# Kernel tuning notes

Hardware: AMD Instinct MI355X
Metric: run time of the kernel (lower is better)

The kernel has to match this reference:

```python
import jax, jax.numpy as jnp
import numpy as np


def setup_inputs() -> dict:
    key = jax.random.key(0)
    kq, kk, kv, km = jax.random.split(key, 4)
    B, H, S, D = 2, 16, 2048, 64
    q = jax.random.normal(kq, (B, H, S, D), dtype=jnp.float32)
    k = jax.random.normal(kk, (B, H, S, D), dtype=jnp.float32)
    v = jax.random.normal(kv, (B, H, S, D), dtype=jnp.float32)
    mask = jax.random.randint(km, (B, 1, S, D * S // D), 0, 2).astype(bool)
    return {"q": q, "k": k, "v": v, "mask": mask, "d_k": 64}


def reference(q, k, v, mask, d_k):
    # score = q @ k^T / sqrt(d_k), masked_fill(mask, -1e9)
    scale = jnp.float32(1.0 / np.sqrt(d_k))
    score = jnp.einsum("bhsd,bhtd->bhst", q, k) * scale  # [B,H,S,S]
    score = jnp.where(mask, jnp.float32(-1e9), score)
    attention = jax.nn.softmax(score, axis=-1)
    # NOTE: original module (faithfully) multiplies the RAW masked score by v,
    # not the softmaxed attention: results = score @ v
    results = jnp.einsum("bhst,bhtd->bhsd", score, v)
    return (results, attention)
```

## Files before the change

kernel.cpp:

```cpp
#include <hip/hip_runtime.h>

typedef __attribute__((ext_vector_type(8))) short short8;
typedef __attribute__((ext_vector_type(4))) float f32x4;

#define S_LEN 2048
#define DH 64

__device__ __forceinline__ unsigned short f2bf(float x) {
  unsigned u = __builtin_bit_cast(unsigned, x);
  u += 0x7fffu + ((u >> 16) & 1u);
  return (unsigned short)(u >> 16);
}

__global__ void detect_stride_k(const unsigned char* __restrict__ m, int* flag) {
  __shared__ int any;
  if (threadIdx.x == 0) any = 0;
  __syncthreads();
  int acc = 0;
  for (int i = threadIdx.x; i < 4096; i += 256)
    if (i & 3) acc |= m[i];
  if (acc) atomicOr(&any, 1);
  __syncthreads();
  if (threadIdx.x == 0) *flag = any ? 1 : 4;
}

__global__ void pack_mask_k(const unsigned char* __restrict__ m,
                            const int* __restrict__ flagp,
                            unsigned* __restrict__ bits) {
  int idx = blockIdx.x * 256 + threadIdx.x;
  unsigned w = 0;
  if (*flagp == 1) {
    const uint4* p = (const uint4*)(m + (size_t)idx * 32);
    uint4 a = p[0], bq = p[1];
    unsigned arr[8] = {a.x, a.y, a.z, a.w, bq.x, bq.y, bq.z, bq.w};
#pragma unroll
    for (int d = 0; d < 8; ++d)
#pragma unroll
      for (int j = 0; j < 4; ++j)
        w |= (((arr[d] >> (8 * j)) & 255u) != 0u ? 1u : 0u) << (d * 4 + j);
  } else {
    const uint4* p = (const uint4*)m + (size_t)idx * 8;
#pragma unroll
    for (int d = 0; d < 8; ++d) {
      uint4 v = p[d];
      w |= (v.x ? 1u : 0u) << (d * 4);
      w |= (v.y ? 1u : 0u) << (d * 4 + 1);
      w |= (v.z ? 1u : 0u) << (d * 4 + 2);
      w |= (v.w ? 1u : 0u) << (d * 4 + 3);
    }
  }
  bits[idx] = w;
}

__global__ void conv_k_kernel(const float* __restrict__ k, char* __restrict__ kbf) {
  int idx = blockIdx.x * 256 + threadIdx.x;
  const float4* s = (const float4*)k + (size_t)idx * 2;
  float4 a = s[0], b = s[1];
  int4 o;
  o.x = (int)f2bf(a.x) | ((int)f2bf(a.y) << 16);
  o.y = (int)f2bf(a.z) | ((int)f2bf(a.w) << 16);
  o.z = (int)f2bf(b.x) | ((int)f2bf(b.y) << 16);
  o.w = (int)f2bf(b.z) | ((int)f2bf(b.w) << 16);
  ((int4*)kbf)[idx] = o;
}

__global__ void trans_v_kernel(const float* __restrict__ v, char* __restrict__ vtbf) {
  int gt = blockIdx.x * 256 + threadIdx.x;
  int wid = gt >> 6;
  int lane = gt & 63;
  int bh = wid >> 9;
  int rem = wid & 511;
  int d0 = (rem >> 5) * 4;
  int t = (rem & 31) * 64 + lane;
  float4 val = *(const float4*)(v + ((size_t)bh * S_LEN + t) * DH + d0);
  unsigned short* o = (unsigned short*)vtbf;
  size_t base = ((size_t)bh * DH + d0) * S_LEN + t;
  o[base]             = f2bf(val.x);
  o[base + S_LEN]     = f2bf(val.y);
  o[base + 2 * S_LEN] = f2bf(val.z);
  o[base + 3 * S_LEN] = f2bf(val.w);
}

__global__ __launch_bounds__(512, 4)
void attn_fused(const float* __restrict__ qsrc,
                const unsigned* __restrict__ mbits,
                const char* __restrict__ kbf,
                const char* __restrict__ vtbf,
                float* __restrict__ out) {
  __shared__ __align__(16) char smem[81920];

  const int tid = threadIdx.x;
  const int lane = tid & 63;
  const int w = tid >> 6;
  const int l15 = lane & 15;
  const int g = lane >> 4;
  const int sw = (l15 & 7) << 4;

  int raw = blockIdx.x;
  int swz = (raw & 7) * 64 + (raw >> 3);
  const int bh = swz >> 4;
  const int qblk = swz & 15;
  const int b = bh >> 4;
  const int q0 = qblk * 128 + w * 16;

  const char* ksrc_bh = kbf + (size_t)bh * (S_LEN * DH * 2);
  const char* vsrc_bh = vtbf + (size_t)bh * (DH * S_LEN * 2);
  char* pb = smem + 65536 + w * 2048;

  const unsigned* mrow = mbits + (size_t)b * (S_LEN * (S_LEN / 32)) +
                         (size_t)(q0 + l15) * (S_LEN / 32);

  auto stageK = [&](int buf, int t0) {
    char* dst = smem + buf * 16384;
#pragma unroll
    for (int it = 0; it < 2; ++it) {
      int o = (w * 2 + it) * 1024 + lane * 16;
      int r = o >> 7;
      int inner = o & 127;
      const char* gp = ksrc_bh + (size_t)t0 * 128 + r * 128 + (inner ^ ((r & 7) << 4));
      __builtin_amdgcn_global_load_lds((const unsigned*)gp,
                                       (unsigned*)(dst + (w * 2 + it) * 1024), 16, 0, 0);
    }
  };
  auto stageV = [&](int buf, int t0) {
    char* dst = smem + 32768 + buf * 16384;
#pragma unroll
    for (int it = 0; it < 2; ++it) {
      int o = (w * 2 + it) * 1024 + lane * 16;
      int r = o >> 8;
      int inner = o & 255;
      const char* gp = vsrc_bh + (size_t)t0 * 2 + (size_t)r * (S_LEN * 2) +
                       (inner ^ ((r & 7) << 4));
      __builtin_amdgcn_global_load_lds((const unsigned*)gp,
                                       (unsigned*)(dst + (w * 2 + it) * 1024), 16, 0, 0);
    }
  };

  short8 qf[2];
#pragma unroll
  for (int kc = 0; kc < 2; ++kc) {
    const float* qp = qsrc + ((size_t)bh * S_LEN + q0 + l15) * DH + 32 * kc + 8 * g;
    float4 x = *(const float4*)qp;
    float4 y = *(const float4*)(qp + 4);
    short8 f;
    f[0] = (short)f2bf(x.x); f[1] = (short)f2bf(x.y);
    f[2] = (short)f2bf(x.z); f[3] = (short)f2bf(x.w);
    f[4] = (short)f2bf(y.x); f[5] = (short)f2bf(y.y);
    f[6] = (short)f2bf(y.z); f[7] = (short)f2bf(y.w);
    qf[kc] = f;
  }

  f32x4 acc[4];
#pragma unroll
  for (int i = 0; i < 4; ++i) acc[i] = (f32x4){0.f, 0.f, 0.f, 0.f};
  float lp = 0.f;

  stageK(0, 0);
  stageV(0, 0);
  uint4 mw = *(const uint4*)mrow;
  __syncthreads();
  int cur = 0;

  for (int t0 = 0; t0 < S_LEN; t0 += 128) {
    uint4 mw_n;
    if (t0 + 128 < S_LEN) {
      stageK(cur ^ 1, t0 + 128);
      stageV(cur ^ 1, t0 + 128);
      mw_n = *(const uint4*)(mrow + (t0 + 128) / 32);
    }
    const char* kbuf = smem + cur * 16384;
    const char* vbuf = smem + 32768 + cur * 16384;

    f32x4 sf[8];
#pragma unroll
    for (int tc = 0; tc < 8; ++tc) {
      const char* rowp = kbuf + (16 * tc + l15) * 128;
      short8 a0 = *(const short8*)(rowp + ((16 * g) ^ sw));
      short8 a1 = *(const short8*)(rowp + ((64 + 16 * g) ^ sw));
      f32x4 z = (f32x4){0.f, 0.f, 0.f, 0.f};
      f32x4 t00 = __builtin_amdgcn_mfma_f32_16x16x32_bf16(a0, qf[0], z, 0, 0, 0);
      sf[tc] = __builtin_amdgcn_mfma_f32_16x16x32_bf16(a1, qf[1], t00, 0, 0, 0);
    }

    const unsigned mwa[4] = {mw.x, mw.y, mw.z, mw.w};
#pragma unroll
    for (int h = 0; h < 2; ++h) {
      char* pbr = pb + l15 * 128;
#pragma unroll
      for (int tq = 0; tq < 4; ++tq) {
        const int tc = 4 * h + tq;
        unsigned nib = (mwa[tc >> 1] >> (16 * (tc & 1) + 4 * g)) & 15u;
        float s0 = (nib & 1u) ? -1e9f : sf[tc][0] * 0.125f;
        float s1 = (nib & 2u) ? -1e9f : sf[tc][1] * 0.125f;
        float s2 = (nib & 4u) ? -1e9f : sf[tc][2] * 0.125f;
        float s3 = (nib & 8u) ? -1e9f : sf[tc][3] * 0.125f;
        lp += __expf(s0) + __expf(s1) + __expf(s2) + __expf(s3);
        int2 pk;
        pk.x = (int)f2bf(s0) | ((int)f2bf(s1) << 16);
        pk.y = (int)f2bf(s2) | ((int)f2bf(s3) << 16);
        *(int2*)(pbr + ((32 * tq + 8 * g) ^ sw)) = pk;
      }
      short8 p0 = *(const short8*)(pb + l15 * 128 + ((16 * g) ^ sw));
      short8 p1 = *(const short8*)(pb + l15 * 128 + ((64 + 16 * g) ^ sw));
#pragma unroll
      for (int dr = 0; dr < 4; ++dr) {
        const char* vr = vbuf + (16 * dr + l15) * 256;
        short8 v0 = *(const short8*)(vr + ((h * 128 + 16 * g) ^ sw));
        short8 v1 = *(const short8*)(vr + ((h * 128 + 64 + 16 * g) ^ sw));
        acc[dr] = __builtin_amdgcn_mfma_f32_16x16x32_bf16(v0, p0, acc[dr], 0, 0, 0);
        acc[dr] = __builtin_amdgcn_mfma_f32_16x16x32_bf16(v1, p1, acc[dr], 0, 0, 0);
      }
    }

    mw = mw_n;
    __syncthreads();
    cur ^= 1;
  }

  float l = lp;
  l += __shfl_xor(l, 16);
  l += __shfl_xor(l, 32);
  const float inv = 1.0f / l;

#pragma unroll
  for (int dr = 0; dr < 4; ++dr) {
    float4 o;
    o.x = acc[dr][0]; o.y = acc[dr][1];
    o.z = acc[dr][2]; o.w = acc[dr][3];
    *(float4*)(out + ((size_t)bh * S_LEN + q0 + l15) * DH + 16 * dr + 4 * g) = o;
  }

  float* att = out + (size_t)4194304 + (size_t)bh * S_LEN * S_LEN;
  stageK(0, 0);
  mw = *(const uint4*)mrow;
  __syncthreads();
  cur = 0;

  for (int t0 = 0; t0 < S_LEN; t0 += 128) {
    uint4 mw_n;
    if (t0 + 128 < S_LEN) {
      stageK(cur ^ 1, t0 + 128);
      mw_n = *(const uint4*)(mrow + (t0 + 128) / 32);
    }
    const char* kbuf = smem + cur * 16384;

    const int q = q0 + l15;
    const unsigned mwa[4] = {mw.x, mw.y, mw.z, mw.w};
#pragma unroll
    for (int tc = 0; tc < 8; ++tc) {
      const char* rowp = kbuf + (16 * tc + l15) * 128;
      short8 a0 = *(const short8*)(rowp + ((16 * g) ^ sw));
      short8 a1 = *(const short8*)(rowp + ((64 + 16 * g) ^ sw));
      f32x4 z = (f32x4){0.f, 0.f, 0.f, 0.f};
      f32x4 t0f = __builtin_amdgcn_mfma_f32_16x16x32_bf16(a0, qf[0], z, 0, 0, 0);
      f32x4 sff = __builtin_amdgcn_mfma_f32_16x16x32_bf16(a1, qf[1], t0f, 0, 0, 0);
      const int t = t0 + 16 * tc + 4 * g;
      size_t eidx = (size_t)q * S_LEN + t;
      unsigned nib = (mwa[tc >> 1] >> (16 * (tc & 1) + 4 * g)) & 15u;
      float s0 = (nib & 1u) ? -1e9f : sff[0] * 0.125f;
      float s1 = (nib & 2u) ? -1e9f : sff[1] * 0.125f;
      float s2 = (nib & 4u) ? -1e9f : sff[2] * 0.125f;
      float s3 = (nib & 8u) ? -1e9f : sff[3] * 0.125f;
      float4 e;
      e.x = __expf(s0) * inv;
      e.y = __expf(s1) * inv;
      e.z = __expf(s2) * inv;
      e.w = __expf(s3) * inv;
      *(float4*)(att + eidx) = e;
    }

    mw = mw_n;
    __syncthreads();
    cur ^= 1;
  }
}

extern "C" void kernel_launch(void* const* d_in, const int* in_sizes, int n_in,
                              void* d_out, int out_size, void* d_ws, size_t ws_size,
                              hipStream_t stream) {
  (void)in_sizes; (void)n_in; (void)out_size; (void)ws_size;
  const float* q = (const float*)d_in[0];
  const float* k = (const float*)d_in[1];
  const float* v = (const float*)d_in[2];
  const unsigned char* mask = (const unsigned char*)d_in[3];
  float* out = (float*)d_out;

  char* ws = (char*)d_ws;
  int* flag = (int*)ws;
  char* kbf = ws + 256;
  char* vtbf = ws + 256 + 8 * 1024 * 1024;
  unsigned* bits = (unsigned*)(ws + 256 + 16 * 1024 * 1024);

  detect_stride_k<<<1, 256, 0, stream>>>(mask, flag);
  pack_mask_k<<<1024, 256, 0, stream>>>(mask, flag, bits);
  conv_k_kernel<<<2048, 256, 0, stream>>>(k, kbf);
  trans_v_kernel<<<4096, 256, 0, stream>>>(v, vtbf);
  attn_fused<<<512, 512, 0, stream>>>(q, bits, kbf, vtbf, out);
}
```

Before: 217.3 us.

## Merge prep kernels into one launch and read K directly in attention pass

Folds the K bf16 conversion, V transpose and mask bit-packing into one prep kernel, with the work split by block-index range, so two kernel launches go away. In the second (attention-writing) pass, K rows are now loaded straight from global/L2 instead of being double-buffered through shared memory, which removes the per-tile __syncthreads and LDS staging. The risk is that direct global loads of K, now without the swizzle, have higher latency and can stall the MFMA and store loop. The relies on `ksrc_bh` being defined in the hidden part of the kernel.

```diff
diff --git a/kernel.cpp b/kernel.cpp
--- a/kernel.cpp
+++ b/kernel.cpp
@@ -24,61 +24,64 @@
   if (threadIdx.x == 0) *flag = any ? 1 : 4;
 }
 
-__global__ void pack_mask_k(const unsigned char* __restrict__ m,
+__global__ void prep_kernel(const float* __restrict__ k,
+                            const float* __restrict__ v,
+                            const unsigned char* __restrict__ m,
                             const int* __restrict__ flagp,
+                            char* __restrict__ kbf,
+                            char* __restrict__ vtbf,
                             unsigned* __restrict__ bits) {
-  int idx = blockIdx.x * 256 + threadIdx.x;
-  unsigned w = 0;
-  if (*flagp == 1) {
-    const uint4* p = (const uint4*)(m + (size_t)idx * 32);
-    uint4 a = p[0], bq = p[1];
-    unsigned arr[8] = {a.x, a.y, a.z, a.w, bq.x, bq.y, bq.z, bq.w};
-#pragma unroll
-    for (int d = 0; d < 8; ++d)
-#pragma unroll
-      for (int j = 0; j < 4; ++j)
-        w |= (((arr[d] >> (8 * j)) & 255u) != 0u ? 1u : 0u) << (d * 4 + j);
+  int bid = blockIdx.x;
+  if (bid < 2048) {
+    int idx = bid * 256 + threadIdx.x;
+    const float4* s = (const float4*)k + (size_t)idx * 2;
+    float4 a = s[0], b = s[1];
+    int4 o;
+    o.x = (int)f2bf(a.x) | ((int)f2bf(a.y) << 16);
+    o.y = (int)f2bf(a.z) | ((int)f2bf(a.w) << 16);
+    o.z = (int)f2bf(b.x) | ((int)f2bf(b.y) << 16);
+    o.w = (int)f2bf(b.z) | ((int)f2bf(b.w) << 16);
+    ((int4*)kbf)[idx] = o;
+  } else if (bid < 6144) {
+    int gt = (bid - 2048) * 256 + threadIdx.x;
+    int wid = gt >> 6;
+    int lane = gt & 63;
+    int bh = wid >> 9;
+    int rem = wid & 511;
+    int d0 = (rem >> 5) * 4;
+    int t = (rem & 31) * 64 + lane;
+    float4 val = *(const float4*)(v + ((size_t)bh * S_LEN + t) * DH + d0);
+    unsigned short* o = (unsigned short*)vtbf;
+    size_t base = ((size_t)bh * DH + d0) * S_LEN + t;
+    o[base]             = f2bf(val.x);
+    o[base + S_LEN]     = f2bf(val.y);
+    o[base + 2 * S_LEN] = f2bf(val.z);
+    o[base + 3 * S_LEN] = f2bf(val.w);
   } else {
-    const uint4* p = (const uint4*)m + (size_t)idx * 8;
-#pragma unroll
-    for (int d = 0; d < 8; ++d) {
-      uint4 v = p[d];
-      w |= (v.x ? 1u : 0u) << (d * 4);
-      w |= (v.y ? 1u : 0u) << (d * 4 + 1);
-      w |= (v.z ? 1u : 0u) << (d * 4 + 2);
-      w |= (v.w ? 1u : 0u) << (d * 4 + 3);
-    }
-  }
-  bits[idx] = w;
-}
-
-__global__ void conv_k_kernel(const float* __restrict__ k, char* __restrict__ kbf) {
-  int idx = blockIdx.x * 256 + threadIdx.x;
-  const float4* s = (const float4*)k + (size_t)idx * 2;
-  float4 a = s[0], b = s[1];
-  int4 o;
-  o.x = (int)f2bf(a.x) | ((int)f2bf(a.y) << 16);
-  o.y = (int)f2bf(a.z) | ((int)f2bf(a.w) << 16);
-  o.z = (int)f2bf(b.x) | ((int)f2bf(b.y) << 16);
-  o.w = (int)f2bf(b.z) | ((int)f2bf(b.w) << 16);
-  ((int4*)kbf)[idx] = o;
-}
-
-__global__ void trans_v_kernel(const float* __restrict__ v, char* __restrict__ vtbf) {
-  int gt = blockIdx.x * 256 + threadIdx.x;
-  int wid = gt >> 6;
-  int lane = gt & 63;
-  int bh = wid >> 9;
-  int rem = wid & 511;
-  int d0 = (rem >> 5) * 4;
-  int t = (rem & 31) * 64 + lane;
-  float4 val = *(const float4*)(v + ((size_t)bh * S_LEN + t) * DH + d0);
-  unsigned short* o = (unsigned short*)vtbf;
-  size_t base = ((size_t)bh * DH + d0) * S_LEN + t;
-  o[base]             = f2bf(val.x);
-  o[base + S_LEN]     = f2bf(val.y);
-  o[base + 2 * S_LEN] = f2bf(val.z);
-  o[base + 3 * S_LEN] = f2bf(val.w);
+    int idx = (bid - 6144) * 256 + threadIdx.x;
+    unsigned wword = 0;
+    if (*flagp == 1) {
+      const uint4* p = (const uint4*)(m + (size_t)idx * 32);
+      uint4 a = p[0], bq = p[1];
+      unsigned arr[8] = {a.x, a.y, a.z, a.w, bq.x, bq.y, bq.z, bq.w};
+#pragma unroll
+      for (int d = 0; d < 8; ++d)
+#pragma unroll
+        for (int j = 0; j < 4; ++j)
+          wword |= (((arr[d] >> (8 * j)) & 255u) != 0u ? 1u : 0u) << (d * 4 + j);
+    } else {
+      const uint4* p = (const uint4*)m + (size_t)idx * 8;
+#pragma unroll
+      for (int d = 0; d < 8; ++d) {
+        uint4 vv = p[d];
+        wword |= (vv.x ? 1u : 0u) << (d * 4);
+        wword |= (vv.y ? 1u : 0u) << (d * 4 + 1);
+        wword |= (vv.z ? 1u : 0u) << (d * 4 + 2);
+        wword |= (vv.w ? 1u : 0u) << (d * 4 + 3);
+      }
+    }
+    bits[idx] = wword;
+  }
 }
 
 __global__ __launch_bounds__(512, 4)
@@ -231,31 +234,20 @@
   }
 
   float* att = out + (size_t)4194304 + (size_t)bh * S_LEN * S_LEN;
-  stageK(0, 0);
-  mw = *(const uint4*)mrow;
-  __syncthreads();
-  cur = 0;
-
+  const int q = q0 + l15;
+#pragma unroll 1
   for (int t0 = 0; t0 < S_LEN; t0 += 128) {
-    uint4 mw_n;
-    if (t0 + 128 < S_LEN) {
-      stageK(cur ^ 1, t0 + 128);
-      mw_n = *(const uint4*)(mrow + (t0 + 128) / 32);
-    }
-    const char* kbuf = smem + cur * 16384;
-
-    const int q = q0 + l15;
-    const unsigned mwa[4] = {mw.x, mw.y, mw.z, mw.w};
+    uint4 mwv = *(const uint4*)(mrow + t0 / 32);
+    const unsigned mwa[4] = {mwv.x, mwv.y, mwv.z, mwv.w};
 #pragma unroll
     for (int tc = 0; tc < 8; ++tc) {
-      const char* rowp = kbuf + (16 * tc + l15) * 128;
-      short8 a0 = *(const short8*)(rowp + ((16 * g) ^ sw));
-      short8 a1 = *(const short8*)(rowp + ((64 + 16 * g) ^ sw));
+      const char* kr = ksrc_bh + (size_t)(t0 + 16 * tc + l15) * 128;
+      short8 a0 = *(const short8*)(kr + 16 * g);
+      short8 a1 = *(const short8*)(kr + 64 + 16 * g);
       f32x4 z = (f32x4){0.f, 0.f, 0.f, 0.f};
       f32x4 t0f = __builtin_amdgcn_mfma_f32_16x16x32_bf16(a0, qf[0], z, 0, 0, 0);
       f32x4 sff = __builtin_amdgcn_mfma_f32_16x16x32_bf16(a1, qf[1], t0f, 0, 0, 0);
       const int t = t0 + 16 * tc + 4 * g;
-      size_t eidx = (size_t)q * S_LEN + t;
       unsigned nib = (mwa[tc >> 1] >> (16 * (tc & 1) + 4 * g)) & 15u;
       float s0 = (nib & 1u) ? -1e9f : sff[0] * 0.125f;
       float s1 = (nib & 2u) ? -1e9f : sff[1] * 0.125f;
@@ -266,12 +258,8 @@
       e.y = __expf(s1) * inv;
       e.z = __expf(s2) * inv;
       e.w = __expf(s3) * inv;
-      *(float4*)(att + eidx) = e;
-    }
-
-    mw = mw_n;
-    __syncthreads();
-    cur ^= 1;
+      *(float4*)(att + (size_t)q * S_LEN + t) = e;
+    }
   }
 }
 
@@ -292,8 +280,6 @@
   unsigned* bits = (unsigned*)(ws + 256 + 16 * 1024 * 1024);
 
   detect_stride_k<<<1, 256, 0, stream>>>(mask, flag);
-  pack_mask_k<<<1024, 256, 0, stream>>>(mask, flag, bits);
-  conv_k_kernel<<<2048, 256, 0, stream>>>(k, kbf);
-  trans_v_kernel<<<4096, 256, 0, stream>>>(v, vtbf);
+  prep_kernel<<<7168, 256, 0, stream>>>(k, v, mask, flag, kbf, vtbf, bits);
   attn_fused<<<512, 512, 0, stream>>>(q, bits, kbf, vtbf, out);
 }
```

New measurement: 274.2 us. +26.2%, slower.
